# Optimization experiments

Measured on AMD Instinct MI355X. Metric: run time of the kernel, lower is better.

Reference implementation:

```python
import jax, jax.numpy as jnp
import numpy as np

ALPHA = 2.0   # spikingjelly surrogate.ATan default alpha
TAU = 2.0
VTH = 1.0     # LIFNode default v_threshold
LN_EPS = 1e-5

@jax.custom_vjp
def atan_spike(x):
    return (x >= 0.).astype(x.dtype)

def _sp_fwd(x):
    return (x >= 0.).astype(x.dtype), x

def _sp_bwd(x, g):
    return (g * (ALPHA / 2.) / (1. + (jnp.pi / 2. * ALPHA * x) ** 2),)

atan_spike.defvjp(_sp_fwd, _sp_bwd)

def lif_step(v, x):
    # spikingjelly LIFNode: decay_input=True, v_reset=0.0 (hard reset)
    h = v + (x - v) / TAU
    s = atan_spike(h - VTH)
    return h * (1. - s), s

def _linear_params(key, fan_in, fan_out):
    k1, k2 = jax.random.split(key)
    bound = 1.0 / np.sqrt(fan_in)
    W = jax.random.uniform(k1, (fan_in, fan_out), jnp.float32, -bound, bound)
    b = jax.random.uniform(k2, (fan_out,), jnp.float32, -bound, bound)
    return W, b

def setup_inputs():
    N, T, C, H, NC = 256, 100, 700, 1024, 20
    ks = jax.random.split(jax.random.key(0), 8)
    x = jax.random.normal(ks[0], (N, T, C), jnp.float32)
    W_in, b_in = _linear_params(ks[1], C, H)
    W_rec, b_rec = _linear_params(ks[2], H, H)
    W2, b2 = _linear_params(ks[3], H, H)
    W3, b3 = _linear_params(ks[4], H, H)
    ln_g = jnp.ones((H,), jnp.float32)
    ln_b = jnp.zeros((H,), jnp.float32)
    W_out, b_out = _linear_params(ks[5], H, NC)
    return dict(x=x, W_in=W_in, b_in=b_in, W_rec=W_rec, b_rec=b_rec,
                W2=W2, b2=b2, W3=W3, b3=b3, ln_g=ln_g, ln_b=ln_b,
                W_out=W_out, b_out=b_out)

def reference(x, W_in, b_in, W_rec, b_rec, W2, b2, W3, b3, ln_g, ln_b, W_out, b_out):
    N, T, C = x.shape
    H = W_in.shape[1]
    # input projection batched over all timesteps: [T, N, H]
    xin = jnp.einsum('ntc,ch->tnh', x, W_in) + b_in
    v0 = jnp.zeros((N, H), x.dtype)

    def step(carry, xin_t):
        v1, v2, s_last = carry
        # Dropout(p=0.5) on spikes_last is eval-mode identity
        inp = xin_t + s_last @ W_rec + b_rec
        v1, s1 = lif_step(v1, inp)
        v2, feat = lif_step(v2, s1 @ W2 + b2)
        return (v1, v2, s1), feat

    _, features = jax.lax.scan(step, (v0, v0, v0), xin)  # [T, N, H]

    # part2: Linear -> LayerNorm (batched over T), then LIF (stateful over T), Dropout(eval)=id, Linear
    y = jnp.einsum('tnh,hk->tnk', features, W3) + b3
    mu = y.mean(-1, keepdims=True)
    var = ((y - mu) ** 2).mean(-1, keepdims=True)
    y = (y - mu) * jax.lax.rsqrt(var + LN_EPS) * ln_g + ln_b

    _, spikes3 = jax.lax.scan(lif_step, v0, y)  # [T, N, H]
    out = jnp.einsum('tnh,hc->tnc', spikes3, W_out) + b_out  # [T, N, num_classes]
    return out.mean(0)
```

## Files before the change

### kernel.cpp

```cpp
#include <hip/hip_runtime.h>

#define T_STEPS 100
#define NB 256
#define CIN 700
#define CINP 704
#define HID 1024
#define NCLS 20
#define NH (NB * HID)
#define TNH ((long)T_STEPS * NH)

typedef __attribute__((ext_vector_type(8))) short bf16x8;
typedef __attribute__((ext_vector_type(4))) float f32x4;

__device__ inline unsigned short f2bf(float f) {
  union { float f; unsigned int u; } c; c.f = f;
  unsigned int u = c.u;
  unsigned int r = (u + 0x7FFFu + ((u >> 16) & 1u)) >> 16;
  return (unsigned short)r;
}
__device__ inline float bf2f(unsigned short h) {
  union { unsigned int u; float f; } c; c.u = ((unsigned int)h) << 16; return c.f;
}
__device__ inline f32x4 mfma16(bf16x8 a, bf16x8 b, f32x4 c) {
  return __builtin_amdgcn_mfma_f32_16x16x32_bf16(a, b, c, 0, 0, 0);
}

__global__ __launch_bounds__(256) void split_w(
    const float* __restrict__ W, unsigned short* __restrict__ oh,
    unsigned short* __restrict__ om, unsigned short* __restrict__ ol,
    int K, int KP) {
  __shared__ float s[32][33];
  const int k0 = blockIdx.x * 32, n0 = blockIdx.y * 32;
  const int tx = threadIdx.x & 31, ty = threadIdx.x >> 5;
#pragma unroll
  for (int i = 0; i < 4; ++i) {
    int k = k0 + ty + 8 * i;
    s[ty + 8 * i][tx] = (k < K) ? W[(long)k * HID + n0 + tx] : 0.f;
  }
  __syncthreads();
#pragma unroll
  for (int i = 0; i < 4; ++i) {
    int n = n0 + ty + 8 * i;
    float f = s[tx][ty + 8 * i];
    unsigned short h = f2bf(f);
    float r1 = f - bf2f(h);
    unsigned short m = f2bf(r1);
    float r2 = r1 - bf2f(m);
    unsigned short l = f2bf(r2);
    long o = (long)n * KP + k0 + tx;
    oh[o] = h; om[o] = m; ol[o] = l;
  }
}

__global__ __launch_bounds__(256) void gemm_sw3(
    const unsigned short* __restrict__ A, const unsigned short* __restrict__ Bh,
    const unsigned short* __restrict__ Bm, const unsigned short* __restrict__ Bl,
    const float* __restrict__ bias, float* __restrict__ out, int M) {
  __shared__ unsigned short As[128][40], Bhs[128][40], Bms[128][40],
      Bls[128][40];
  const int tid = threadIdx.x;
  const int w = tid >> 6, lane = tid & 63;
  const int wm = w >> 1, wn = w & 1;
  const int l15 = lane & 15, g = lane >> 4;
  const long row0 = (long)blockIdx.x * 128;
  const int col0 = blockIdx.y * 128;
  f32x4 acc[4][4];
  const f32x4 zf = {0.f, 0.f, 0.f, 0.f};
#pragma unroll
  for (int mi = 0; mi < 4; ++mi)
#pragma unroll
    for (int ni = 0; ni < 4; ++ni) acc[mi][ni] = zf;

  for (int kt = 0; kt < HID; kt += 32) {
#pragma unroll
    for (int i = 0; i < 2; ++i) {
      int slot = tid + 256 * i;
      int r = slot >> 2, kk = (slot & 3) * 8;
      *(uint4*)&As[r][kk] = *(const uint4*)(A + (row0 + r) * HID + kt + kk);
      long gi = (long)(col0 + r) * HID + kt + kk;
      *(uint4*)&Bhs[r][kk] = *(const uint4*)(Bh + gi);
      *(uint4*)&Bms[r][kk] = *(const uint4*)(Bm + gi);
      *(uint4*)&Bls[r][kk] = *(const uint4*)(Bl + gi);
    }
    __syncthreads();
    bf16x8 af[4];
#pragma unroll
    for (int mi = 0; mi < 4; ++mi)
      af[mi] = *(const bf16x8*)&As[wm * 64 + mi * 16 + l15][g * 8];
#pragma unroll
    for (int ni = 0; ni < 4; ++ni) {
      int r = wn * 64 + ni * 16 + l15;
      bf16x8 bb;
      bb = *(const bf16x8*)&Bhs[r][g * 8];
#pragma unroll
      for (int mi = 0; mi < 4; ++mi) acc[mi][ni] = mfma16(af[mi], bb, acc[mi][ni]);
      bb = *(const bf16x8*)&Bms[r][g * 8];
#pragma unroll
      for (int mi = 0; mi < 4; ++mi) acc[mi][ni] = mfma16(af[mi], bb, acc[mi][ni]);
      bb = *(const bf16x8*)&Bls[r][g * 8];
#pragma unroll
      for (int mi = 0; mi < 4; ++mi) acc[mi][ni] = mfma16(af[mi], bb, acc[mi][ni]);
    }
    __syncthreads();
  }
#pragma unroll
  for (int mi = 0; mi < 4; ++mi)
#pragma unroll
    for (int ni = 0; ni < 4; ++ni) {
      int c = col0 + wn * 64 + ni * 16 + l15;
      float b = bias[c];
#pragma unroll
      for (int reg = 0; reg < 4; ++reg) {
        long r = row0 + wm * 64 + mi * 16 + g * 4 + reg;
        out[r * HID + c] = acc[mi][ni][reg] + b;
      }
    }
}

__global__ __launch_bounds__(256) void gemm_x6(
    const float* __restrict__ X, const unsigned short* __restrict__ Bh,
    const unsigned short* __restrict__ Bm, const unsigned short* __restrict__ Bl,
    const float* __restrict__ bias, float* __restrict__ out) {
  __shared__ unsigned short Ahs[128][40], Ams[128][40], Als[128][40];
  __shared__ unsigned short Bhs[128][40], Bms[128][40], Bls[128][40];
  const int tid = threadIdx.x;
  const int w = tid >> 6, lane = tid & 63;
  const int wm = w >> 1, wn = w & 1;
  const int l15 = lane & 15, g = lane >> 4;
  const long row0 = (long)blockIdx.x * 128;
  const int col0 = blockIdx.y * 128;
  f32x4 acc[4][4];
  const f32x4 zf = {0.f, 0.f, 0.f, 0.f};
#pragma unroll
  for (int mi = 0; mi < 4; ++mi)
#pragma unroll
    for (int ni = 0; ni < 4; ++ni) acc[mi][ni] = zf;

  for (int kt = 0; kt < CINP; kt += 32) {
#pragma unroll
    for (int i = 0; i < 4; ++i) {
      int slot = tid + 256 * i;
      int r = slot >> 3, kq = (slot & 7) * 4;
      float4 v = make_float4(0.f, 0.f, 0.f, 0.f);
      if (kt + kq < CIN) v = *(const float4*)(X + (row0 + r) * (long)CIN + kt + kq);
      unsigned int h0, h1, m0, m1, l0, l1;
      {
        float f0 = v.x, f1 = v.y;
        unsigned short a = f2bf(f0), b = f2bf(f1);
        float ra = f0 - bf2f(a), rb = f1 - bf2f(b);
        unsigned short c = f2bf(ra), d = f2bf(rb);
        float sa = ra - bf2f(c), sb = rb - bf2f(d);
        h0 = (unsigned int)a | ((unsigned int)b << 16);
        m0 = (unsigned int)c | ((unsigned int)d << 16);
        l0 = (unsigned int)f2bf(sa) | ((unsigned int)f2bf(sb) << 16);
      }
      {
        float f0 = v.z, f1 = v.w;
        unsigned short a = f2bf(f0), b = f2bf(f1);
        float ra = f0 - bf2f(a), rb = f1 - bf2f(b);
        unsigned short c = f2bf(ra), d = f2bf(rb);
        float sa = ra - bf2f(c), sb = rb - bf2f(d);
        h1 = (unsigned int)a | ((unsigned int)b << 16);
        m1 = (unsigned int)c | ((unsigned int)d << 16);
        l1 = (unsigned int)f2bf(sa) | ((unsigned int)f2bf(sb) << 16);
      }
      uint2 uh = {h0, h1}, um = {m0, m1}, ul = {l0, l1};
      *(uint2*)&Ahs[r][kq] = uh;
      *(uint2*)&Ams[r][kq] = um;
      *(uint2*)&Als[r][kq] = ul;
    }
#pragma unroll
    for (int i = 0; i < 2; ++i) {
      int slot = tid + 256 * i;
      int r = slot >> 2, kk = (slot & 3) * 8;
      long gi = (long)(col0 + r) * CINP + kt + kk;
      *(uint4*)&Bhs[r][kk] = *(const uint4*)(Bh + gi);
      *(uint4*)&Bms[r][kk] = *(const uint4*)(Bm + gi);
      *(uint4*)&Bls[r][kk] = *(const uint4*)(Bl + gi);
    }
    __syncthreads();
    bf16x8 ah[4], am[4], al[4];
#pragma unroll
    for (int mi = 0; mi < 4; ++mi) {
      int r = wm * 64 + mi * 16 + l15;
      ah[mi] = *(const bf16x8*)&Ahs[r][g * 8];
      am[mi] = *(const bf16x8*)&Ams[r][g * 8];
      al[mi] = *(const bf16x8*)&Als[r][g * 8];
    }
#pragma unroll
    for (int ni = 0; ni < 4; ++ni) {
      int r = wn * 64 + ni * 16 + l15;
      bf16x8 bb;
      bb = *(const bf16x8*)&Bhs[r][g * 8];
#pragma unroll
      for (int mi = 0; mi < 4; ++mi) acc[mi][ni] = mfma16(ah[mi], bb, acc[mi][ni]);
#pragma unroll
      for (int mi = 0; mi < 4; ++mi) acc[mi][ni] = mfma16(am[mi], bb, acc[mi][ni]);
#pragma unroll
      for (int mi = 0; mi < 4; ++mi) acc[mi][ni] = mfma16(al[mi], bb, acc[mi][ni]);
      bb = *(const bf16x8*)&Bms[r][g * 8];
#pragma unroll
      for (int mi = 0; mi < 4; ++mi) acc[mi][ni] = mfma16(ah[mi], bb, acc[mi][ni]);
#pragma unroll
      for (int mi = 0; mi < 4; ++mi) acc[mi][ni] = mfma16(am[mi], bb, acc[mi][ni]);
      bb = *(const bf16x8*)&Bls[r][g * 8];
#pragma unroll
      for (int mi = 0; mi < 4; ++mi) acc[mi][ni] = mfma16(ah[mi], bb, acc[mi][ni]);
    }
    __syncthreads();
  }
#pragma unroll
  for (int mi = 0; mi < 4; ++mi)
#pragma unroll
    for (int ni = 0; ni < 4; ++ni) {
      int c = col0 + wn * 64 + ni * 16 + l15;
      float b = bias[c];
#pragma unroll
      for (int reg = 0; reg < 4; ++reg) {
        long r = row0 + wm * 64 + mi * 16 + g * 4 + reg;
        int t = (int)(r % T_STEPS);
        int n = (int)(r / T_STEPS);
        out[((long)t * NB + n) * HID + c] = acc[mi][ni][reg] + b;
      }
    }
}

__global__ __launch_bounds__(256) void step_mfma(
    const unsigned short* __restrict__ Sprev,
    const unsigned short* __restrict__ Bh, const unsigned short* __restrict__ Bm,
    const unsigned short* __restrict__ Bl, const float* __restrict__ b_rec,
    const float* __restrict__ xin_t, float* __restrict__ v1,
    unsigned short* __restrict__ Sout) {
  __shared__ unsigned short As[64][72], Bhs[64][72], Bms[64][72], Bls[64][72];
  const int tid = threadIdx.x;
  const int w = tid >> 6, lane = tid & 63;
  const int wm = w >> 1, wn = w & 1;
  const int l15 = lane & 15, g = lane >> 4;
  const int row0 = blockIdx.x * 64;
  const int col0 = blockIdx.y * 64;
  f32x4 acc[2][2];
  const f32x4 zf = {0.f, 0.f, 0.f, 0.f};
#pragma unroll
  for (int mi = 0; mi < 2; ++mi)
#pragma unroll
    for (int ni = 0; ni < 2; ++ni) acc[mi][ni] = zf;

  for (int kt = 0; kt < HID; kt += 64) {
#pragma unroll
    for (int i = 0; i < 2; ++i) {
      int slot = tid + 256 * i;
      int r = slot >> 3, kk = (slot & 7) * 8;
      *(uint4*)&As[r][kk] = *(const uint4*)(Sprev + (long)(row0 + r) * HID + kt + kk);
      long gi = (long)(col0 + r) * HID + kt + kk;
      *(uint4*)&Bhs[r][kk] = *(const uint4*)(Bh + gi);
      *(uint4*)&Bms[r][kk] = *(const uint4*)(Bm + gi);
      *(uint4*)&Bls[r][kk] = *(const uint4*)(Bl + gi);
    }
    __syncthreads();
#pragma unroll
    for (int ks = 0; ks < 2; ++ks) {
      bf16x8 af[2];
#pragma unroll
      for (int mi = 0; mi < 2; ++mi)
        af[mi] = *(const bf16x8*)&As[wm * 32 + mi * 16 + l15][ks * 32 + g * 8];
#pragma unroll
      for (int ni = 0; ni < 2; ++ni) {
        int r = wn * 32 + ni * 16 + l15;
        bf16x8 bb;
        bb = *(const bf16x8*)&Bhs[r][ks * 32 + g * 8];
#pragma unroll
        for (int mi = 0; mi < 2; ++mi) acc[mi][ni] = mfma16(af[mi], bb, acc[mi][ni]);
        bb = *(const bf16x8*)&Bms[r][ks * 32 + g * 8];
#pragma unroll
        for (int mi = 0; mi < 2; ++mi) acc[mi][ni] = mfma16(af[mi], bb, acc[mi][ni]);
        bb = *(const bf16x8*)&Bls[r][ks * 32 + g * 8];
#pragma unroll
        for (int mi = 0; mi < 2; ++mi) acc[mi][ni] = mfma16(af[mi], bb, acc[mi][ni]);
      }
    }
    __syncthreads();
  }
#pragma unroll
  for (int mi = 0; mi < 2; ++mi)
#pragma unroll
    for (int ni = 0; ni < 2; ++ni) {
      int c = col0 + wn * 32 + ni * 16 + l15;
      float br = b_rec[c];
#pragma unroll
      for (int reg = 0; reg < 4; ++reg) {
        int n = row0 + wm * 32 + mi * 16 + g * 4 + reg;
        long idx = (long)n * HID + c;
        float inp = acc[mi][ni][reg] + br + xin_t[idx];
        float v = v1[idx];
        float h = v + (inp - v) * 0.5f;
        bool sp = (h >= 1.0f);
        v1[idx] = sp ? 0.0f : h;
        Sout[idx] = sp ? 0x3F80u : 0u;
      }
    }
}

__global__ __launch_bounds__(256) void lif_prologue(
    const float* __restrict__ xin0, const float* __restrict__ b_rec,
    float* __restrict__ v1, unsigned short* __restrict__ s0) {
  long id = (long)blockIdx.x * 256 + threadIdx.x;
  float inp = xin0[id] + b_rec[id & (HID - 1)];
  float h = inp * 0.5f;
  bool sp = (h >= 1.0f);
  v1[id] = sp ? 0.0f : h;
  s0[id] = sp ? 0x3F80u : 0u;
}

__global__ __launch_bounds__(256) void lif2_kernel(
    const float* __restrict__ z, unsigned short* __restrict__ feat) {
  long id = (long)blockIdx.x * 256 + threadIdx.x;
  float v = 0.0f;
  for (int t = 0; t < T_STEPS; ++t) {
    float x = z[(long)t * NH + id];
    float h = v + (x - v) * 0.5f;
    bool sp = (h >= 1.0f);
    v = sp ? 0.0f : h;
    feat[(long)t * NH + id] = sp ? 0x3F80u : 0u;
  }
}

__global__ __launch_bounds__(256) void ln_kernel(float* __restrict__ y,
                                                 const float* __restrict__ g,
                                                 const float* __restrict__ b) {
  __shared__ float red[4];
  long row = blockIdx.x;
  float* p = y + row * HID;
  int tid = threadIdx.x;
  float x[4];
#pragma unroll
  for (int i = 0; i < 4; ++i) x[i] = p[tid + 256 * i];
  float s = x[0] + x[1] + x[2] + x[3];
#pragma unroll
  for (int m = 32; m; m >>= 1) s += __shfl_xor(s, m, 64);
  if ((tid & 63) == 0) red[tid >> 6] = s;
  __syncthreads();
  float mu = (red[0] + red[1] + red[2] + red[3]) * (1.0f / HID);
  __syncthreads();
  float r0 = x[0] - mu, r1 = x[1] - mu, r2 = x[2] - mu, r3 = x[3] - mu;
  float v = r0 * r0 + r1 * r1 + r2 * r2 + r3 * r3;
#pragma unroll
  for (int m = 32; m; m >>= 1) v += __shfl_xor(v, m, 64);
  if ((tid & 63) == 0) red[tid >> 6] = v;
  __syncthreads();
  float var = (red[0] + red[1] + red[2] + red[3]) * (1.0f / HID);
  float inv = 1.0f / sqrtf(var + 1e-5f);
#pragma unroll
  for (int i = 0; i < 4; ++i) {
    int h = tid + 256 * i;
    p[h] = (x[i] - mu) * inv * g[h] + b[h];
  }
}

__global__ __launch_bounds__(256) void lifc_kernel(
    const float* __restrict__ y, float* __restrict__ sbar) {
  long id = (long)blockIdx.x * 256 + threadIdx.x;
  float v = 0.0f, acc = 0.0f;
  for (int t = 0; t < T_STEPS; ++t) {
    float x = y[(long)t * NH + id];
    float h = v + (x - v) * 0.5f;
    if (h >= 1.0f) {
      acc += 1.0f;
      v = 0.0f;
    } else {
      v = h;
    }
  }
  sbar[id] = acc * (1.0f / T_STEPS);
}

__global__ __launch_bounds__(64) void out_kernel(
    const float* __restrict__ sbar, const float* __restrict__ Wout,
    const float* __restrict__ bout, float* __restrict__ out) {
  int n = blockIdx.x, j = threadIdx.x;
  if (j >= NCLS) return;
  const float* s = sbar + (long)n * HID;
  float a0 = 0.f, a1 = 0.f, a2 = 0.f, a3 = 0.f;
  for (int k = 0; k < HID; k += 4) {
    a0 += s[k + 0] * Wout[(k + 0) * NCLS + j];
    a1 += s[k + 1] * Wout[(k + 1) * NCLS + j];
    a2 += s[k + 2] * Wout[(k + 2) * NCLS + j];
    a3 += s[k + 3] * Wout[(k + 3) * NCLS + j];
  }
  out[n * NCLS + j] = ((a0 + a1) + (a2 + a3)) + bout[j];
}

extern "C" void kernel_launch(void* const* d_in, const int* in_sizes, int n_in,
                              void* d_out, int out_size, void* d_ws,
                              size_t ws_size, hipStream_t stream) {
  const float* x = (const float*)d_in[0];
  const float* W_in = (const float*)d_in[1];
  const float* b_in = (const float*)d_in[2];
  const float* W_rec = (const float*)d_in[3];
  const float* b_rec = (const float*)d_in[4];
  const float* W2 = (const float*)d_in[5];
  const float* b2 = (const float*)d_in[6];
  const float* W3 = (const float*)d_in[7];
  const float* b3 = (const float*)d_in[8];
  const float* ln_g = (const float*)d_in[9];
  const float* ln_b = (const float*)d_in[10];
  const float* W_out = (const float*)d_in[11];
  const float* b_out = (const float*)d_in[12];
  float* out = (float*)d_out;
  (void)in_sizes; (void)n_in; (void)out_size; (void)ws_size;

  char* ws = (char*)d_ws;
  size_t off = 0;
  auto carve = [&](size_t bytes) -> void* {
    void* p = (void*)(ws + off);
    off += (bytes + 255) & ~(size_t)255;
    return p;
  };
  unsigned short* wih = (unsigned short*)carve((size_t)HID * CINP * 2);
  unsigned short* wim = (unsigned short*)carve((size_t)HID * CINP * 2);
  unsigned short* wil = (unsigned short*)carve((size_t)HID * CINP * 2);
  unsigned short* wrh = (unsigned short*)carve((size_t)HID * HID * 2);
  unsigned short* wrm = (unsigned short*)carve((size_t)HID * HID * 2);
  unsigned short* wrl = (unsigned short*)carve((size_t)HID * HID * 2);
  unsigned short* w2h = (unsigned short*)carve((size_t)HID * HID * 2);
  unsigned short* w2m = (unsigned short*)carve((size_t)HID * HID * 2);
  unsigned short* w2l = (unsigned short*)carve((size_t)HID * HID * 2);
  unsigned short* w3h = (unsigned short*)carve((size_t)HID * HID * 2);
  unsigned short* w3m = (unsigned short*)carve((size_t)HID * HID * 2);
  unsigned short* w3l = (unsigned short*)carve((size_t)HID * HID * 2);
  float* xin = (float*)carve((size_t)TNH * 4);
  unsigned short* s1 = (unsigned short*)carve((size_t)TNH * 2);
  float* v1 = (float*)carve((size_t)NH * 4);
  float* sbar = (float*)carve((size_t)NH * 4);

  split_w<<<dim3(CINP / 32, HID / 32), 256, 0, stream>>>(W_in, wih, wim, wil, CIN, CINP);
  split_w<<<dim3(HID / 32, HID / 32), 256, 0, stream>>>(W_rec, wrh, wrm, wrl, HID, HID);
  split_w<<<dim3(HID / 32, HID / 32), 256, 0, stream>>>(W2, w2h, w2m, w2l, HID, HID);
  split_w<<<dim3(HID / 32, HID / 32), 256, 0, stream>>>(W3, w3h, w3m, w3l, HID, HID);

  gemm_x6<<<dim3(25600 / 128, HID / 128), 256, 0, stream>>>(x, wih, wim, wil, b_in, xin);

  lif_prologue<<<dim3(NH / 256), 256, 0, stream>>>(xin, b_rec, v1, s1);
  for (int t = 1; t < T_STEPS; ++t) {
    step_mfma<<<dim3(NB / 64, HID / 64), 256, 0, stream>>>(
        s1 + (size_t)(t - 1) * NH, wrh, wrm, wrl, b_rec, xin + (size_t)t * NH,
        v1, s1 + (size_t)t * NH);
  }

  gemm_sw3<<<dim3(25600 / 128, HID / 128), 256, 0, stream>>>(s1, w2h, w2m, w2l, b2, xin, 25600);
  lif2_kernel<<<dim3(NH / 256), 256, 0, stream>>>(xin, s1);

  gemm_sw3<<<dim3(25600 / 128, HID / 128), 256, 0, stream>>>(s1, w3h, w3m, w3l, b3, xin, 25600);
  ln_kernel<<<dim3(25600), 256, 0, stream>>>(xin, ln_g, ln_b);
  lifc_kernel<<<dim3(NH / 256), 256, 0, stream>>>(xin, sbar);
  out_kernel<<<dim3(NB), 64, 0, stream>>>(sbar, W_out, b_out, out);
}
```

Baseline: 2.886 ms.

## Replace per-timestep recurrent launches with persistent scan kernel using grid barrier

The 99 separate step_mfma launches are replaced by one persistent kernel of 256 blocks that loops over all timesteps. Blocks synchronise through an atomic counter barrier in global memory, and each thread keeps its LIF membrane state in registers, so the v1 global buffer goes away. Each block stages a full 32-row slab of the previous spikes in LDS and streams its weight columns straight from global/L2. This targets launch overhead and global round trips for state, but it depends on all 256 blocks being co-resident, and the spin barrier has a timeout that could silently break correctness.

```diff
diff --git a/kernel.cpp b/kernel.cpp
--- a/kernel.cpp
+++ b/kernel.cpp
@@ -225,90 +225,99 @@
     }
 }
 
-__global__ __launch_bounds__(256) void step_mfma(
-    const unsigned short* __restrict__ Sprev,
+__device__ inline void bar_arrive(int* cnt) {
+  __threadfence();
+  __syncthreads();
+  if (threadIdx.x == 0)
+    __hip_atomic_fetch_add(cnt, 1, __ATOMIC_RELEASE, __HIP_MEMORY_SCOPE_AGENT);
+}
+__device__ inline void bar_wait(int* cnt, int target) {
+  if (threadIdx.x == 0) {
+    int spins = 0;
+    while (__hip_atomic_load(cnt, __ATOMIC_ACQUIRE, __HIP_MEMORY_SCOPE_AGENT) <
+               target &&
+           spins < 200000) {
+      __builtin_amdgcn_s_sleep(2);
+      ++spins;
+    }
+  }
+  __syncthreads();
+  __threadfence();
+}
+
+__global__ __launch_bounds__(256) void scan_kernel(
     const unsigned short* __restrict__ Bh, const unsigned short* __restrict__ Bm,
     const unsigned short* __restrict__ Bl, const float* __restrict__ b_rec,
-    const float* __restrict__ xin_t, float* __restrict__ v1,
-    unsigned short* __restrict__ Sout) {
-  __shared__ unsigned short As[64][72], Bhs[64][72], Bms[64][72], Bls[64][72];
+    const float* __restrict__ xin, unsigned short* __restrict__ s1,
+    int* __restrict__ bar) {
+  __shared__ unsigned short As[32][1032];
   const int tid = threadIdx.x;
   const int w = tid >> 6, lane = tid & 63;
-  const int wm = w >> 1, wn = w & 1;
+  const int wr = w >> 1, wc = w & 1;
   const int l15 = lane & 15, g = lane >> 4;
-  const int row0 = blockIdx.x * 64;
-  const int col0 = blockIdx.y * 64;
-  f32x4 acc[2][2];
-  const f32x4 zf = {0.f, 0.f, 0.f, 0.f};
-#pragma unroll
-  for (int mi = 0; mi < 2; ++mi)
-#pragma unroll
-    for (int ni = 0; ni < 2; ++ni) acc[mi][ni] = zf;
-
-  for (int kt = 0; kt < HID; kt += 64) {
-#pragma unroll
-    for (int i = 0; i < 2; ++i) {
+  const int row0 = blockIdx.x * 32;
+  const int col0 = blockIdx.y * 32;
+  const int myrow16 = row0 + wr * 16;
+  const int mycol = col0 + wc * 16 + l15;
+  const float brc = b_rec[mycol];
+  const unsigned short* bhp = Bh + (long)mycol * HID;
+  const unsigned short* bmp = Bm + (long)mycol * HID;
+  const unsigned short* blp = Bl + (long)mycol * HID;
+  const int arow = wr * 16 + l15;
+
+  f32x4 v1 = {0.f, 0.f, 0.f, 0.f};
+
+#pragma unroll
+  for (int reg = 0; reg < 4; ++reg) {
+    int n = myrow16 + g * 4 + reg;
+    float inp = xin[(long)n * HID + mycol] + brc;
+    float h = inp * 0.5f;
+    bool sp = (h >= 1.0f);
+    v1[reg] = sp ? 0.0f : h;
+    s1[(long)n * HID + mycol] = sp ? 0x3F80u : 0u;
+  }
+  bar_arrive(bar);
+
+  for (int t = 1; t < T_STEPS; ++t) {
+    bar_wait(bar, 256 * t);
+    const unsigned short* sp_prev = s1 + (size_t)(t - 1) * NH;
+#pragma unroll
+    for (int i = 0; i < 16; ++i) {
       int slot = tid + 256 * i;
-      int r = slot >> 3, kk = (slot & 7) * 8;
-      *(uint4*)&As[r][kk] = *(const uint4*)(Sprev + (long)(row0 + r) * HID + kt + kk);
-      long gi = (long)(col0 + r) * HID + kt + kk;
-      *(uint4*)&Bhs[r][kk] = *(const uint4*)(Bh + gi);
-      *(uint4*)&Bms[r][kk] = *(const uint4*)(Bm + gi);
-      *(uint4*)&Bls[r][kk] = *(const uint4*)(Bl + gi);
+      int r = slot >> 7, k8 = (slot & 127) << 3;
+      *(uint4*)&As[r][k8] =
+          *(const uint4*)(sp_prev + (long)(row0 + r) * HID + k8);
     }
     __syncthreads();
-#pragma unroll
-    for (int ks = 0; ks < 2; ++ks) {
-      bf16x8 af[2];
-#pragma unroll
-      for (int mi = 0; mi < 2; ++mi)
-        af[mi] = *(const bf16x8*)&As[wm * 32 + mi * 16 + l15][ks * 32 + g * 8];
-#pragma unroll
-      for (int ni = 0; ni < 2; ++ni) {
-        int r = wn * 32 + ni * 16 + l15;
-        bf16x8 bb;
-        bb = *(const bf16x8*)&Bhs[r][ks * 32 + g * 8];
-#pragma unroll
-        for (int mi = 0; mi < 2; ++mi) acc[mi][ni] = mfma16(af[mi], bb, acc[mi][ni]);
-        bb = *(const bf16x8*)&Bms[r][ks * 32 + g * 8];
-#pragma unroll
-        for (int mi = 0; mi < 2; ++mi) acc[mi][ni] = mfma16(af[mi], bb, acc[mi][ni]);
-        bb = *(const bf16x8*)&Bls[r][ks * 32 + g * 8];
-#pragma unroll
-        for (int mi = 0; mi < 2; ++mi) acc[mi][ni] = mfma16(af[mi], bb, acc[mi][ni]);
-      }
-    }
-    __syncthreads();
-  }
-#pragma unroll
-  for (int mi = 0; mi < 2; ++mi)
-#pragma unroll
-    for (int ni = 0; ni < 2; ++ni) {
-      int c = col0 + wn * 32 + ni * 16 + l15;
-      float br = b_rec[c];
-#pragma unroll
-      for (int reg = 0; reg < 4; ++reg) {
-        int n = row0 + wm * 32 + mi * 16 + g * 4 + reg;
-        long idx = (long)n * HID + c;
-        float inp = acc[mi][ni][reg] + br + xin_t[idx];
-        float v = v1[idx];
-        float h = v + (inp - v) * 0.5f;
-        bool sp = (h >= 1.0f);
-        v1[idx] = sp ? 0.0f : h;
-        Sout[idx] = sp ? 0x3F80u : 0u;
-      }
-    }
-}
-
-__global__ __launch_bounds__(256) void lif_prologue(
-    const float* __restrict__ xin0, const float* __restrict__ b_rec,
-    float* __restrict__ v1, unsigned short* __restrict__ s0) {
-  long id = (long)blockIdx.x * 256 + threadIdx.x;
-  float inp = xin0[id] + b_rec[id & (HID - 1)];
-  float h = inp * 0.5f;
-  bool sp = (h >= 1.0f);
-  v1[id] = sp ? 0.0f : h;
-  s0[id] = sp ? 0x3F80u : 0u;
+    const float* xp = xin + (size_t)t * NH;
+    float xv[4];
+#pragma unroll
+    for (int reg = 0; reg < 4; ++reg)
+      xv[reg] = xp[(long)(myrow16 + g * 4 + reg) * HID + mycol];
+
+    f32x4 acc = {0.f, 0.f, 0.f, 0.f};
+#pragma unroll 4
+    for (int kt = 0; kt < HID; kt += 32) {
+      bf16x8 af = *(const bf16x8*)&As[arow][kt + g * 8];
+      bf16x8 b0 = *(const bf16x8*)(bhp + kt + g * 8);
+      bf16x8 b1 = *(const bf16x8*)(bmp + kt + g * 8);
+      bf16x8 b2 = *(const bf16x8*)(blp + kt + g * 8);
+      acc = mfma16(af, b0, acc);
+      acc = mfma16(af, b1, acc);
+      acc = mfma16(af, b2, acc);
+    }
+    unsigned short* so = s1 + (size_t)t * NH;
+#pragma unroll
+    for (int reg = 0; reg < 4; ++reg) {
+      int n = myrow16 + g * 4 + reg;
+      float inp = acc[reg] + brc + xv[reg];
+      float h = v1[reg] + (inp - v1[reg]) * 0.5f;
+      bool sp = (h >= 1.0f);
+      v1[reg] = sp ? 0.0f : h;
+      so[(long)n * HID + mycol] = sp ? 0x3F80u : 0u;
+    }
+    if (t < T_STEPS - 1) bar_arrive(bar);
+  }
 }
 
 __global__ __launch_bounds__(256) void lif2_kernel(
@@ -429,8 +438,8 @@
   unsigned short* w3l = (unsigned short*)carve((size_t)HID * HID * 2);
   float* xin = (float*)carve((size_t)TNH * 4);
   unsigned short* s1 = (unsigned short*)carve((size_t)TNH * 2);
-  float* v1 = (float*)carve((size_t)NH * 4);
   float* sbar = (float*)carve((size_t)NH * 4);
+  int* bar = (int*)carve(256);
 
   split_w<<<dim3(CINP / 32, HID / 32), 256, 0, stream>>>(W_in, wih, wim, wil, CIN, CINP);
   split_w<<<dim3(HID / 32, HID / 32), 256, 0, stream>>>(W_rec, wrh, wrm, wrl, HID, HID);
@@ -439,12 +448,8 @@
 
   gemm_x6<<<dim3(25600 / 128, HID / 128), 256, 0, stream>>>(x, wih, wim, wil, b_in, xin);
 
-  lif_prologue<<<dim3(NH / 256), 256, 0, stream>>>(xin, b_rec, v1, s1);
-  for (int t = 1; t < T_STEPS; ++t) {
-    step_mfma<<<dim3(NB / 64, HID / 64), 256, 0, stream>>>(
-        s1 + (size_t)(t - 1) * NH, wrh, wrm, wrl, b_rec, xin + (size_t)t * NH,
-        v1, s1 + (size_t)t * NH);
-  }
+  hipMemsetAsync(bar, 0, 256, stream);
+  scan_kernel<<<dim3(8, 32), 256, 0, stream>>>(wrh, wrm, wrl, b_rec, xin, s1, bar);
 
   gemm_sw3<<<dim3(25600 / 128, HID / 128), 256, 0, stream>>>(s1, w2h, w2m, w2l, b2, xin, 25600);
   lif2_kernel<<<dim3(NH / 256), 256, 0, stream>>>(xin, s1);
```

Measured after the change: 7.340 ms. 154% more time.
